# Kernel tuning notes

Hardware: AMD Instinct MI355X
Metric: run time of the kernel (lower is better)

Reference implementation:

```python
import jax, jax.numpy as jnp
import numpy as np

B, N, K, CIN, COUT = 2, 8192, 16, 64, 64


def setup_inputs() -> dict:
    key = jax.random.key(0)
    ks = jax.random.split(key, 12)
    w = lambda k, shape: jax.random.normal(k, shape, jnp.float32) * 0.02
    return dict(
        pos=jax.random.normal(ks[0], (B, N, 3), jnp.float32),
        features=jax.random.normal(ks[1], (B, N, CIN), jnp.float32),
        emb_w=w(ks[2], (CIN, COUT)), emb_b=jnp.zeros((COUT,), jnp.float32),
        wq=w(ks[3], (COUT, COUT)), wk=w(ks[4], (COUT, COUT)), wv=w(ks[5], (COUT, COUT)),
        pe_w1=w(ks[6], (3, COUT)), pe_b1=jnp.zeros((COUT,), jnp.float32),
        pe_w2=w(ks[7], (COUT, COUT)), pe_b2=jnp.zeros((COUT,), jnp.float32),
        at_w1=w(ks[8], (COUT, COUT)), at_b1=jnp.zeros((COUT,), jnp.float32),
        at_w2=w(ks[9], (COUT, COUT)), at_b2=jnp.zeros((COUT,), jnp.float32),
        out_w=w(ks[10], (COUT, CIN)), out_b=jnp.zeros((CIN,), jnp.float32),
    )


def _gather(x, idx):
    # x: [B, N, C], idx: [B, N, K] -> [B, N, K, C]
    return jax.vmap(lambda xb, ib: xb[ib])(x, idx)


def reference(pos, features, emb_w, emb_b, wq, wk, wv,
              pe_w1, pe_b1, pe_w2, pe_b2,
              at_w1, at_b1, at_w2, at_b2, out_w, out_b):
    # KNN: squared pairwise distances, take k smallest (includes self)
    sq = jnp.sum(pos * pos, axis=-1)                                  # [B, N]
    d2 = sq[:, :, None] + sq[:, None, :] - 2.0 * jnp.einsum('bnd,bmd->bnm', pos, pos)
    _, knn_idx = jax.lax.top_k(-d2, K)                                # [B, N, K]

    # recenter_groups: neighbor positions relative to query point
    grouped_pos = _gather(pos, knn_idx) - pos[:, :, None, :]          # [B, N, K, 3]

    x = features @ emb_w + emb_b                                      # [B, N, COUT]
    q = x @ wq                                                        # [B, N, COUT]
    k = _gather(x @ wk, knn_idx)                                      # [B, N, K, COUT]
    v = _gather(x @ wv, knn_idx)                                      # [B, N, K, COUT]

    # mlp_posenc: Linear(3,C) -> ReLU -> Linear(C,C)
    posenc = jax.nn.relu(grouped_pos @ pe_w1 + pe_b1) @ pe_w2 + pe_b2  # [B, N, K, COUT]

    # mlp_attn on (q - k + posenc), softmax over neighbor axis (dim=-2)
    h = q[:, :, None, :] - k + posenc
    attn = jax.nn.relu(h @ at_w1 + at_b1) @ at_w2 + at_b2
    attn = jax.nn.softmax(attn / np.float32(np.sqrt(COUT)), axis=-2)

    result = jnp.einsum('bmnf,bmnf->bmf', attn, v + posenc)           # [B, N, COUT]
    return result @ out_w + out_b + features                          # [B, N, CIN]
```

## Files before the change

### kernel.cpp

```cpp
#include <hip/hip_runtime.h>
#include <hip/hip_bf16.h>

#define BB 2
#define NN 8192
#define SPL 16
#define CAND (NN/SPL)
#define NPTS (BB*NN)

#define PART_OFF 0u
#define IDX_OFF  4194304u
#define WT_OFF   4456448u
#define QB_OFF   0u
#define KVB_OFF  1048576u

typedef __attribute__((ext_vector_type(8))) short bf16x8;
typedef __attribute__((ext_vector_type(4))) float f32x4;

__device__ __forceinline__ unsigned umn(unsigned a, unsigned b) {
#if __has_builtin(__builtin_elementwise_min)
  return __builtin_elementwise_min(a, b);
#else
  return a < b ? a : b;
#endif
}
__device__ __forceinline__ unsigned umx(unsigned a, unsigned b) {
#if __has_builtin(__builtin_elementwise_max)
  return __builtin_elementwise_max(a, b);
#else
  return a < b ? b : a;
#endif
}

__device__ inline unsigned short f2bf(float x) {
  __hip_bfloat16 b = __float2bfloat16(x);
  return *(unsigned short*)&b;
}

#define HCOL(c, j) ((((((c) >> 3) + (j)) & 7) << 3) | ((c) & 7))

__global__ __launch_bounds__(256) void k1_knn(const float* __restrict__ pos,
                                              unsigned* __restrict__ part)
{
  const int tid = threadIdx.x;
  const int g = blockIdx.x * 256 + tid;
  const int s = blockIdx.y;
  const int bu = __builtin_amdgcn_readfirstlane(g >> 13);
  const float qx = pos[g * 3 + 0], qy = pos[g * 3 + 1], qz = pos[g * 3 + 2];
  const float* __restrict__ cp = pos + (bu * NN + s * CAND) * 3;
  const unsigned jb = (unsigned)(s * CAND);
  unsigned m[16];
#pragma unroll
  for (int i = 0; i < 16; i++) m[i] = 0xFFFFFFFFu;

  constexpr int OE8[19][2] = {
    {0,1},{2,3},{4,5},{6,7},
    {0,2},{1,3},{4,6},{5,7},
    {1,2},{5,6},
    {0,4},{1,5},{2,6},{3,7},
    {2,4},{3,5},
    {1,2},{3,4},{5,6}
  };

  for (int j0 = 0; j0 < CAND; j0 += 8) {
    float c[24];
#pragma unroll
    for (int i = 0; i < 24; i++) c[i] = cp[j0 * 3 + i];
    unsigned b[8];
#pragma unroll
    for (int i = 0; i < 8; i++) {
      float dx = c[i * 3 + 0] - qx;
      float dy = c[i * 3 + 1] - qy;
      float dz = c[i * 3 + 2] - qz;
      float d2 = fmaf(dx, dx, fmaf(dy, dy, dz * dz));
      b[i] = (__float_as_uint(d2) & 0xFFFFE000u) | (jb + (unsigned)(j0 + i));
    }
#pragma unroll
    for (int cc = 0; cc < 19; cc++) {
      const int x = OE8[cc][0], y = OE8[cc][1];
      unsigned lo = umn(b[x], b[y]);
      unsigned hi = umx(b[x], b[y]);
      b[x] = hi; b[y] = lo;
    }
#pragma unroll
    for (int i = 0; i < 8; i++) m[8 + i] = umn(m[8 + i], b[i]);
#pragma unroll
    for (int d = 8; d; d >>= 1) {
#pragma unroll
      for (int i = 0; i < 16; i++) {
        if ((i & d) == 0) {
          const int l = i | d;
          unsigned lo = umn(m[i], m[l]);
          unsigned hi = umx(m[i], m[l]);
          m[i] = lo; m[l] = hi;
        }
      }
    }
  }
#pragma unroll
  for (int i = 0; i < 16; i++)
    part[(unsigned)(s * 16 + i) * NPTS + (unsigned)g] = m[i];
}

__global__ __launch_bounds__(256) void k2_merge(
    const unsigned* __restrict__ part, int* __restrict__ knn_idx,
    const float* __restrict__ pe_w2, const float* __restrict__ at_w1,
    const float* __restrict__ at_w2, const float* __restrict__ out_w,
    unsigned short* __restrict__ wt)
{
  if (blockIdx.x >= 64) {
    const int t = (blockIdx.x - 64) * 256 + threadIdx.x;
    const float* s;
    switch (t >> 12) {
      case 0: s = pe_w2; break;
      case 1: s = at_w1; break;
      case 2: s = at_w2; break;
      default: s = out_w; break;
    }
    const int idx = t & 4095, f = idx >> 6, c = idx & 63;
    wt[t] = f2bf(s[c * 64 + f]);
    return;
  }
  const int g = blockIdx.x * 256 + threadIdx.x;
  unsigned run[16];
#pragma unroll
  for (int i = 0; i < 16; i++) run[i] = part[i * NPTS + g];
#pragma unroll
  for (int l = 1; l < SPL; l++) {
#pragma unroll
    for (int i = 0; i < 16; i++)
      run[i] = umn(run[i], part[(l * 16 + 15 - i) * NPTS + g]);
#pragma unroll
    for (int d = 8; d; d >>= 1) {
#pragma unroll
      for (int i = 0; i < 16; i++) {
        if ((i & d) == 0) {
          const int l2 = i | d;
          unsigned lo = umn(run[i], run[l2]);
          unsigned hi = umx(run[i], run[l2]);
          run[i] = lo; run[l2] = hi;
        }
      }
    }
  }
  const int base = (g >> 13) * NN;
  int outv[16];
#pragma unroll
  for (int i = 0; i < 16; i++) outv[i] = base + (int)(run[i] & 0x1FFFu);
  int4* o = (int4*)(knn_idx + g * 16);
  o[0] = make_int4(outv[0], outv[1], outv[2], outv[3]);
  o[1] = make_int4(outv[4], outv[5], outv[6], outv[7]);
  o[2] = make_int4(outv[8], outv[9], outv[10], outv[11]);
  o[3] = make_int4(outv[12], outv[13], outv[14], outv[15]);
}

__global__ __launch_bounds__(256) void k34_embqkv(
    const float* __restrict__ feat,
    const float* __restrict__ emb_w, const float* __restrict__ emb_b,
    const float* __restrict__ wq, const float* __restrict__ wk,
    const float* __restrict__ wv,
    float* __restrict__ qo, unsigned* __restrict__ kvp)
{
  __shared__ float wl[16384];
  __shared__ float xl[2048];
  for (int i = threadIdx.x; i < 4096; i += 256) {
    wl[i] = emb_w[i];
    wl[4096 + i] = wq[i];
    wl[8192 + i] = wk[i];
    wl[12288 + i] = wv[i];
  }
  const int col = threadIdx.x & 63;
  const int rg = threadIdx.x >> 6;
  const int row0 = blockIdx.x * 32 + rg * 8;
  const int rowu = __builtin_amdgcn_readfirstlane(row0);
  __syncthreads();
  {
    float acc[8];
    float bias = emb_b[col];
#pragma unroll
    for (int r = 0; r < 8; r++) acc[r] = bias;
    for (int c = 0; c < 64; c++) {
      float w = wl[c * 64 + col];
      const float* fp = feat + rowu * 64 + c;
#pragma unroll
      for (int r = 0; r < 8; r++) acc[r] = fmaf(fp[r * 64], w, acc[r]);
    }
#pragma unroll
    for (int r = 0; r < 8; r++) xl[(rg * 8 + r) * 64 + col] = acc[r];
  }
  __syncthreads();
  float aq[8], ak[8], av[8];
#pragma unroll
  for (int r = 0; r < 8; r++) { aq[r] = 0.f; ak[r] = 0.f; av[r] = 0.f; }
  for (int c = 0; c < 64; c++) {
    float w0 = wl[4096 + c * 64 + col];
    float w1 = wl[8192 + c * 64 + col];
    float w2 = wl[12288 + c * 64 + col];
#pragma unroll
    for (int r = 0; r < 8; r++) {
      float xv = xl[(rg * 8 + r) * 64 + c];
      aq[r] = fmaf(xv, w0, aq[r]);
      ak[r] = fmaf(xv, w1, ak[r]);
      av[r] = fmaf(xv, w2, av[r]);
    }
  }
#pragma unroll
  for (int r = 0; r < 8; r++) {
    qo[(row0 + r) * 64 + col] = aq[r];
    kvp[(row0 + r) * 64 + col] =
        ((unsigned)f2bf(av[r]) << 16) | (unsigned)f2bf(ak[r]);
  }
}

__device__ inline void mv(const unsigned short* hm, const bf16x8 B[4][2],
                          const float bias[4], int ln, int s0, int s1,
                          f32x4 acc[4])
{
  bf16x8 a0 = *(const bf16x8*)(hm + ln * 64 + s0);
  bf16x8 a1 = *(const bf16x8*)(hm + ln * 64 + s1);
#pragma unroll
  for (int t = 0; t < 4; t++) {
    f32x4 a = {bias[t], bias[t], bias[t], bias[t]};
    a = __builtin_amdgcn_mfma_f32_16x16x32_bf16(a0, B[t][0], a, 0, 0, 0);
    a = __builtin_amdgcn_mfma_f32_16x16x32_bf16(a1, B[t][1], a, 0, 0, 0);
    acc[t] = a;
  }
}

__global__ __launch_bounds__(256, 2) void k5_attn(
    const float* __restrict__ pos, const float* __restrict__ qg,
    const unsigned* __restrict__ kvp, const float* __restrict__ featf,
    const float* __restrict__ pe_w1, const float* __restrict__ pe_b1,
    const float* __restrict__ pe_b2, const float* __restrict__ at_b1,
    const float* __restrict__ at_b2, const float* __restrict__ out_b,
    const unsigned short* __restrict__ wt, const int* __restrict__ knn,
    float* __restrict__ out)
{
  __shared__ unsigned short hma[4][1024];
  __shared__ unsigned short resm[1024];
  const int tid = threadIdx.x;
  const int wid = tid >> 6, lane = tid & 63;
  const int ln = lane & 15, quad = lane >> 4;
  unsigned short* hm = hma[wid];
  const int s0 = ((quad + ln) & 7) << 3;
  const int s1 = ((4 + quad + ln) & 7) << 3;

  bf16x8 Bf[3][4][2];
#pragma unroll
  for (int m = 0; m < 3; m++)
#pragma unroll
    for (int t = 0; t < 4; t++)
#pragma unroll
      for (int ks = 0; ks < 2; ks++)
        Bf[m][t][ks] = *(const bf16x8*)(wt + m * 4096 + (t * 16 + ln) * 64 +
                                        ks * 32 + quad * 8);
  bf16x8 bo[2];
#pragma unroll
  for (int ks = 0; ks < 2; ks++)
    bo[ks] = *(const bf16x8*)(wt + 3 * 4096 + (wid * 16 + ln) * 64 +
                              ks * 32 + quad * 8);

  float pw10 = pe_w1[lane], pw11 = pe_w1[64 + lane], pw12 = pe_w1[128 + lane];
  float pb1 = pe_b1[lane];
  float bpe[4], ba1[4], ba2[4];
#pragma unroll
  for (int t = 0; t < 4; t++) {
    bpe[t] = pe_b2[t * 16 + ln];
    ba1[t] = at_b1[t * 16 + ln];
    ba2[t] = at_b2[t * 16 + ln];
  }

  const int p0 = blockIdx.x * 16 + wid * 4;
  const int ps0 = __builtin_amdgcn_readfirstlane(p0);
  int4 cur[4];
  {
    const int4* ip4 = (const int4*)(knn + ps0 * 16);
#pragma unroll
    for (int u = 0; u < 4; u++) cur[u] = ip4[u];
  }

  for (int pp = 0; pp < 4; pp++) {
    const int p = p0 + pp;
    const int ps = __builtin_amdgcn_readfirstlane(p);
    int jj[16];
#pragma unroll
    for (int u = 0; u < 4; u++) {
      jj[u*4+0] = cur[u].x; jj[u*4+1] = cur[u].y;
      jj[u*4+2] = cur[u].z; jj[u*4+3] = cur[u].w;
    }
    int4 nxt[4];
    {
      const int pn = (pp < 3) ? (ps + 1) : ps;
      const int4* np4 = (const int4*)(knn + pn * 16);
#pragma unroll
      for (int u = 0; u < 4; u++) nxt[u] = np4[u];
    }
    unsigned kvw[4][4];
#pragma unroll
    for (int r = 0; r < 4; r++) {
      const unsigned* kp = kvp + jj[quad * 4 + r] * 64 + ln;
#pragma unroll
      for (int t = 0; t < 4; t++) kvw[r][t] = kp[t * 16];
    }
    float qv[4];
#pragma unroll
    for (int t = 0; t < 4; t++) qv[t] = qg[p * 64 + t * 16 + ln];

    const float* mp = pos + ps * 3;
    float pnx = mp[0], pny = mp[1], pnz = mp[2];
#pragma unroll
    for (int j = 0; j < 16; j++) {
      const float* np_ = pos + jj[j] * 3;
      float h1 = fmaf(np_[2] - pnz, pw12,
                 fmaf(np_[1] - pny, pw11,
                 fmaf(np_[0] - pnx, pw10, pb1)));
      hm[j * 64 + HCOL(lane, j)] = f2bf(fmaxf(h1, 0.f));
    }
    f32x4 accp[4];
    mv(hm, Bf[0], bpe, ln, s0, s1, accp);
    float vpe[4][4];
#pragma unroll
    for (int r = 0; r < 4; r++) {
      const int j = quad * 4 + r;
#pragma unroll
      for (int t = 0; t < 4; t++) {
        const unsigned w = kvw[r][t];
        float kf = __uint_as_float(w << 16);
        float vf = __uint_as_float(w & 0xFFFF0000u);
        float pe = accp[t][r];
        vpe[t][r] = vf + pe;
        hm[j * 64 + HCOL(t * 16 + ln, j)] = f2bf(qv[t] - kf + pe);
      }
    }
    f32x4 acch[4];
    mv(hm, Bf[1], ba1, ln, s0, s1, acch);
#pragma unroll
    for (int t = 0; t < 4; t++)
#pragma unroll
      for (int r = 0; r < 4; r++) {
        const int j = quad * 4 + r;
        hm[j * 64 + HCOL(t * 16 + ln, j)] = f2bf(fmaxf(acch[t][r], 0.f));
      }
    f32x4 lg[4];
    mv(hm, Bf[2], ba2, ln, s0, s1, lg);
    const int pb = wid * 4 + pp;
#pragma unroll
    for (int t = 0; t < 4; t++) {
      float e0 = __expf(lg[t][0] * 0.125f);
      float e1 = __expf(lg[t][1] * 0.125f);
      float e2 = __expf(lg[t][2] * 0.125f);
      float e3 = __expf(lg[t][3] * 0.125f);
      float ss = (e0 + e1) + (e2 + e3);
      float dt = fmaf(e3, vpe[t][3], fmaf(e2, vpe[t][2],
                 fmaf(e1, vpe[t][1], e0 * vpe[t][0])));
      ss += __shfl_xor(ss, 16); ss += __shfl_xor(ss, 32);
      dt += __shfl_xor(dt, 16); dt += __shfl_xor(dt, 32);
      float res = dt / ss;
      if (quad == 0) resm[pb * 64 + HCOL(t * 16 + ln, pb)] = f2bf(res);
    }
#pragma unroll
    for (int u = 0; u < 4; u++) cur[u] = nxt[u];
  }
  __syncthreads();
  {
    const int nt = wid;
    float ob = out_b[nt * 16 + ln];
    f32x4 acc = {ob, ob, ob, ob};
#pragma unroll
    for (int ks = 0; ks < 2; ks++) {
      bf16x8 a = *(const bf16x8*)(resm + ln * 64 +
                                  (((ks * 4 + quad + ln) & 7) << 3));
      acc = __builtin_amdgcn_mfma_f32_16x16x32_bf16(a, bo[ks], acc, 0, 0, 0);
    }
#pragma unroll
    for (int r = 0; r < 4; r++) {
      const int pt = blockIdx.x * 16 + quad * 4 + r;
      const int f = nt * 16 + ln;
      out[pt * 64 + f] = acc[r] + featf[pt * 64 + f];
    }
  }
}

extern "C" void kernel_launch(void* const* d_in, const int* in_sizes, int n_in,
                              void* d_out, int out_size, void* d_ws, size_t ws_size,
                              hipStream_t stream)
{
  (void)in_sizes; (void)n_in; (void)out_size; (void)ws_size;
  const float* pos   = (const float*)d_in[0];
  const float* feat  = (const float*)d_in[1];
  const float* emb_w = (const float*)d_in[2];
  const float* emb_b = (const float*)d_in[3];
  const float* wq    = (const float*)d_in[4];
  const float* wk    = (const float*)d_in[5];
  const float* wv    = (const float*)d_in[6];
  const float* pe_w1 = (const float*)d_in[7];
  const float* pe_b1 = (const float*)d_in[8];
  const float* pe_w2 = (const float*)d_in[9];
  const float* pe_b2 = (const float*)d_in[10];
  const float* at_w1 = (const float*)d_in[11];
  const float* at_b1 = (const float*)d_in[12];
  const float* at_w2 = (const float*)d_in[13];
  const float* at_b2 = (const float*)d_in[14];
  const float* out_w = (const float*)d_in[15];
  const float* out_b = (const float*)d_in[16];
  float* ws = (float*)d_ws;

  dim3 g1(NPTS / 256, SPL);
  k1_knn<<<g1, 256, 0, stream>>>(pos, (unsigned*)ws + PART_OFF);
  k2_merge<<<128, 256, 0, stream>>>((unsigned*)ws + PART_OFF,
      (int*)ws + IDX_OFF, pe_w2, at_w1, at_w2, out_w,
      (unsigned short*)(ws + WT_OFF));
  k34_embqkv<<<NPTS / 32, 256, 0, stream>>>(feat, emb_w, emb_b, wq, wk, wv,
      ws + QB_OFF, (unsigned*)ws + KVB_OFF);
  k5_attn<<<NPTS / 16, 256, 0, stream>>>(pos, ws + QB_OFF,
      (unsigned*)ws + KVB_OFF, feat, pe_w1, pe_b1, pe_b2, at_b1, at_b2, out_b,
      (unsigned short*)(ws + WT_OFF), (int*)ws + IDX_OFF, (float*)d_out);
}
```

Measured before the change: 240.1 us.

## Fuse four kernels into two and merge KNN partials inside attention kernel

Merges the KNN partial search, embedding/QKV projection and weight transposition into one heterogeneous launch, selected by block index. The KNN top-16 merge moves into the attention kernel, where four lanes per wave compute neighbor indices into shared memory instead of reading a separate index array. The KNN inner loop now sorts 16 candidates per step instead of 8, and positions are repacked as float4 for single-load gathers. This removes two launches and one global round trip for the indices, at the cost of serial merge work on a few lanes, more register pressure in the KNN loop, and lower LDS occupancy in the fused first kernel.

Measured after the change: 249.7 us. +4.0%, slower.

```diff
diff --git a/kernel.cpp b/kernel.cpp
--- a/kernel.cpp
+++ b/kernel.cpp
@@ -7,11 +7,11 @@
 #define CAND (NN/SPL)
 #define NPTS (BB*NN)
 
-#define PART_OFF 0u
-#define IDX_OFF  4194304u
-#define WT_OFF   4456448u
-#define QB_OFF   0u
-#define KVB_OFF  1048576u
+#define POS4_OFF 0u
+#define PART_OFF 65536u
+#define QB_OFF   4259840u
+#define KVB_OFF  5308416u
+#define WT_OFF   6356992u
 
 typedef __attribute__((ext_vector_type(8))) short bf16x8;
 typedef __attribute__((ext_vector_type(4))) float f32x4;
@@ -38,77 +38,144 @@
 
 #define HCOL(c, j) ((((((c) >> 3) + (j)) & 7) << 3) | ((c) & 7))
 
-__global__ __launch_bounds__(256) void k1_knn(const float* __restrict__ pos,
-                                              unsigned* __restrict__ part)
-{
-  const int tid = threadIdx.x;
-  const int g = blockIdx.x * 256 + tid;
-  const int s = blockIdx.y;
-  const int bu = __builtin_amdgcn_readfirstlane(g >> 13);
-  const float qx = pos[g * 3 + 0], qy = pos[g * 3 + 1], qz = pos[g * 3 + 2];
-  const float* __restrict__ cp = pos + (bu * NN + s * CAND) * 3;
-  const unsigned jb = (unsigned)(s * CAND);
-  unsigned m[16];
-#pragma unroll
-  for (int i = 0; i < 16; i++) m[i] = 0xFFFFFFFFu;
-
-  constexpr int OE8[19][2] = {
-    {0,1},{2,3},{4,5},{6,7},
-    {0,2},{1,3},{4,6},{5,7},
-    {1,2},{5,6},
-    {0,4},{1,5},{2,6},{3,7},
-    {2,4},{3,5},
-    {1,2},{3,4},{5,6}
-  };
-
-  for (int j0 = 0; j0 < CAND; j0 += 8) {
-    float c[24];
-#pragma unroll
-    for (int i = 0; i < 24; i++) c[i] = cp[j0 * 3 + i];
-    unsigned b[8];
-#pragma unroll
-    for (int i = 0; i < 8; i++) {
-      float dx = c[i * 3 + 0] - qx;
-      float dy = c[i * 3 + 1] - qy;
-      float dz = c[i * 3 + 2] - qz;
-      float d2 = fmaf(dx, dx, fmaf(dy, dy, dz * dz));
-      b[i] = (__float_as_uint(d2) & 0xFFFFE000u) | (jb + (unsigned)(j0 + i));
-    }
-#pragma unroll
-    for (int cc = 0; cc < 19; cc++) {
-      const int x = OE8[cc][0], y = OE8[cc][1];
-      unsigned lo = umn(b[x], b[y]);
-      unsigned hi = umx(b[x], b[y]);
-      b[x] = hi; b[y] = lo;
-    }
-#pragma unroll
-    for (int i = 0; i < 8; i++) m[8 + i] = umn(m[8 + i], b[i]);
-#pragma unroll
-    for (int d = 8; d; d >>= 1) {
-#pragma unroll
-      for (int i = 0; i < 16; i++) {
-        if ((i & d) == 0) {
-          const int l = i | d;
-          unsigned lo = umn(m[i], m[l]);
-          unsigned hi = umx(m[i], m[l]);
-          m[i] = lo; m[l] = hi;
-        }
-      }
-    }
-  }
-#pragma unroll
-  for (int i = 0; i < 16; i++)
-    part[(unsigned)(s * 16 + i) * NPTS + (unsigned)g] = m[i];
-}
-
-__global__ __launch_bounds__(256) void k2_merge(
-    const unsigned* __restrict__ part, int* __restrict__ knn_idx,
+__global__ __launch_bounds__(256) void mega1(
+    const float* __restrict__ pos, const float* __restrict__ feat,
+    const float* __restrict__ emb_w, const float* __restrict__ emb_b,
+    const float* __restrict__ wq, const float* __restrict__ wk,
+    const float* __restrict__ wv,
     const float* __restrict__ pe_w2, const float* __restrict__ at_w1,
     const float* __restrict__ at_w2, const float* __restrict__ out_w,
-    unsigned short* __restrict__ wt)
+    float* __restrict__ ws)
 {
-  if (blockIdx.x >= 64) {
-    const int t = (blockIdx.x - 64) * 256 + threadIdx.x;
+  __shared__ __align__(16) char smem[57344];
+  const int tid = threadIdx.x;
+  const int bx = blockIdx.x;
+  float* pos4 = ws + POS4_OFF;
+  unsigned* part = (unsigned*)ws + PART_OFF;
+  float* qg = ws + QB_OFF;
+  unsigned* kvp = (unsigned*)ws + KVB_OFF;
+  unsigned short* wt = (unsigned short*)(ws + WT_OFF);
+
+  if (bx < 512) {
+    float* wl = (float*)smem;
+    float* xl = (float*)(smem + 49152);
+    if (tid < 32) {
+      const int p = bx * 32 + tid;
+      float x = pos[p * 3 + 0], y = pos[p * 3 + 1], z = pos[p * 3 + 2];
+      float4 v = {x, y, z, fmaf(x, x, fmaf(y, y, z * z))};
+      ((float4*)pos4)[p] = v;
+    }
+    for (int i = tid; i < 4096; i += 256) wl[i] = emb_w[i];
+    const int col = tid & 63;
+    const int rg = tid >> 6;
+    const int row0 = bx * 32 + rg * 8;
+    const int rowu = __builtin_amdgcn_readfirstlane(row0);
+    __syncthreads();
+    {
+      float acc[8];
+      float bias = emb_b[col];
+#pragma unroll
+      for (int r = 0; r < 8; r++) acc[r] = bias;
+      for (int c = 0; c < 64; c++) {
+        float w = wl[c * 64 + col];
+        const float* fp = feat + rowu * 64 + c;
+#pragma unroll
+        for (int r = 0; r < 8; r++) acc[r] = fmaf(fp[r * 64], w, acc[r]);
+      }
+#pragma unroll
+      for (int r = 0; r < 8; r++) xl[(rg * 8 + r) * 64 + col] = acc[r];
+    }
+    __syncthreads();
+    for (int i = tid; i < 4096; i += 256) {
+      wl[i] = wq[i];
+      wl[4096 + i] = wk[i];
+      wl[8192 + i] = wv[i];
+    }
+    __syncthreads();
+    float aq[8], ak[8], av[8];
+#pragma unroll
+    for (int r = 0; r < 8; r++) { aq[r] = 0.f; ak[r] = 0.f; av[r] = 0.f; }
+    for (int c = 0; c < 64; c++) {
+      float w0 = wl[c * 64 + col];
+      float w1 = wl[4096 + c * 64 + col];
+      float w2 = wl[8192 + c * 64 + col];
+#pragma unroll
+      for (int r = 0; r < 8; r++) {
+        float xv = xl[(rg * 8 + r) * 64 + c];
+        aq[r] = fmaf(xv, w0, aq[r]);
+        ak[r] = fmaf(xv, w1, ak[r]);
+        av[r] = fmaf(xv, w2, av[r]);
+      }
+    }
+#pragma unroll
+    for (int r = 0; r < 8; r++) {
+      qg[(row0 + r) * 64 + col] = aq[r];
+      kvp[(row0 + r) * 64 + col] =
+          ((unsigned)f2bf(av[r]) << 16) | (unsigned)f2bf(ak[r]);
+    }
+  } else if (bx < 1536) {
+    constexpr int OE[63][2] = {
+      {0,1},{2,3},{4,5},{6,7},{8,9},{10,11},{12,13},{14,15},
+      {0,2},{1,3},{4,6},{5,7},{8,10},{9,11},{12,14},{13,15},
+      {1,2},{5,6},{9,10},{13,14},
+      {0,4},{1,5},{2,6},{3,7},{8,12},{9,13},{10,14},{11,15},
+      {2,4},{3,5},{10,12},{11,13},
+      {1,2},{3,4},{5,6},{9,10},{11,12},{13,14},
+      {0,8},{1,9},{2,10},{3,11},{4,12},{5,13},{6,14},{7,15},
+      {4,8},{5,9},{6,10},{7,11},
+      {2,4},{3,5},{6,8},{7,9},{10,12},{11,13},
+      {1,2},{3,4},{5,6},{7,8},{9,10},{11,12},{13,14}
+    };
+    const int vb = bx - 512;
+    const int g = (vb & 63) * 256 + tid;
+    const int s = vb >> 6;
+    const int bu = __builtin_amdgcn_readfirstlane(g >> 13);
+    const float qx = pos[g * 3 + 0], qy = pos[g * 3 + 1], qz = pos[g * 3 + 2];
+    const float* __restrict__ cp = pos + (bu * NN + s * CAND) * 3;
+    const unsigned jb = (unsigned)(s * CAND);
+    unsigned m[16];
+#pragma unroll
+    for (int i = 0; i < 16; i++) m[i] = 0xFFFFFFFFu;
+    for (int j0 = 0; j0 < CAND; j0 += 16) {
+      float c[48];
+#pragma unroll
+      for (int i = 0; i < 48; i++) c[i] = cp[j0 * 3 + i];
+      unsigned b[16];
+#pragma unroll
+      for (int i = 0; i < 16; i++) {
+        float dx = c[i * 3 + 0] - qx;
+        float dy = c[i * 3 + 1] - qy;
+        float dz = c[i * 3 + 2] - qz;
+        float d2 = fmaf(dx, dx, fmaf(dy, dy, dz * dz));
+        b[i] = (__float_as_uint(d2) & 0xFFFFE000u) | (jb + (unsigned)(j0 + i));
+      }
+#pragma unroll
+      for (int cc = 0; cc < 63; cc++) {
+        const int x = OE[cc][0], y = OE[cc][1];
+        unsigned lo = umn(b[x], b[y]);
+        unsigned hi = umx(b[x], b[y]);
+        b[x] = hi; b[y] = lo;
+      }
+#pragma unroll
+      for (int i = 0; i < 16; i++) m[i] = umn(m[i], b[i]);
+#pragma unroll
+      for (int d = 8; d; d >>= 1) {
+#pragma unroll
+        for (int i = 0; i < 16; i++) {
+          if ((i & d) == 0) {
+            const int l = i | d;
+            unsigned lo = umn(m[i], m[l]);
+            unsigned hi = umx(m[i], m[l]);
+            m[i] = lo; m[l] = hi;
+          }
+        }
+      }
+    }
+#pragma unroll
+    for (int i = 0; i < 16; i++)
+      part[(unsigned)(s * 16 + i) * NPTS + (unsigned)g] = m[i];
+  } else {
+    const int t = (bx - 1536) * 256 + tid;
     const float* s;
     switch (t >> 12) {
       case 0: s = pe_w2; break;
@@ -118,96 +185,6 @@
     }
     const int idx = t & 4095, f = idx >> 6, c = idx & 63;
     wt[t] = f2bf(s[c * 64 + f]);
-    return;
-  }
-  const int g = blockIdx.x * 256 + threadIdx.x;
-  unsigned run[16];
-#pragma unroll
-  for (int i = 0; i < 16; i++) run[i] = part[i * NPTS + g];
-#pragma unroll
-  for (int l = 1; l < SPL; l++) {
-#pragma unroll
-    for (int i = 0; i < 16; i++)
-      run[i] = umn(run[i], part[(l * 16 + 15 - i) * NPTS + g]);
-#pragma unroll
-    for (int d = 8; d; d >>= 1) {
-#pragma unroll
-      for (int i = 0; i < 16; i++) {
-        if ((i & d) == 0) {
-          const int l2 = i | d;
-          unsigned lo = umn(run[i], run[l2]);
-          unsigned hi = umx(run[i], run[l2]);
-          run[i] = lo; run[l2] = hi;
-        }
-      }
-    }
-  }
-  const int base = (g >> 13) * NN;
-  int outv[16];
-#pragma unroll
-  for (int i = 0; i < 16; i++) outv[i] = base + (int)(run[i] & 0x1FFFu);
-  int4* o = (int4*)(knn_idx + g * 16);
-  o[0] = make_int4(outv[0], outv[1], outv[2], outv[3]);
-  o[1] = make_int4(outv[4], outv[5], outv[6], outv[7]);
-  o[2] = make_int4(outv[8], outv[9], outv[10], outv[11]);
-  o[3] = make_int4(outv[12], outv[13], outv[14], outv[15]);
-}
-
-__global__ __launch_bounds__(256) void k34_embqkv(
-    const float* __restrict__ feat,
-    const float* __restrict__ emb_w, const float* __restrict__ emb_b,
-    const float* __restrict__ wq, const float* __restrict__ wk,
-    const float* __restrict__ wv,
-    float* __restrict__ qo, unsigned* __restrict__ kvp)
-{
-  __shared__ float wl[16384];
-  __shared__ float xl[2048];
-  for (int i = threadIdx.x; i < 4096; i += 256) {
-    wl[i] = emb_w[i];
-    wl[4096 + i] = wq[i];
-    wl[8192 + i] = wk[i];
-    wl[12288 + i] = wv[i];
-  }
-  const int col = threadIdx.x & 63;
-  const int rg = threadIdx.x >> 6;
-  const int row0 = blockIdx.x * 32 + rg * 8;
-  const int rowu = __builtin_amdgcn_readfirstlane(row0);
-  __syncthreads();
-  {
-    float acc[8];
-    float bias = emb_b[col];
-#pragma unroll
-    for (int r = 0; r < 8; r++) acc[r] = bias;
-    for (int c = 0; c < 64; c++) {
-      float w = wl[c * 64 + col];
-      const float* fp = feat + rowu * 64 + c;
-#pragma unroll
-      for (int r = 0; r < 8; r++) acc[r] = fmaf(fp[r * 64], w, acc[r]);
-    }
-#pragma unroll
-    for (int r = 0; r < 8; r++) xl[(rg * 8 + r) * 64 + col] = acc[r];
-  }
-  __syncthreads();
-  float aq[8], ak[8], av[8];
-#pragma unroll
-  for (int r = 0; r < 8; r++) { aq[r] = 0.f; ak[r] = 0.f; av[r] = 0.f; }
-  for (int c = 0; c < 64; c++) {
-    float w0 = wl[4096 + c * 64 + col];
-    float w1 = wl[8192 + c * 64 + col];
-    float w2 = wl[12288 + c * 64 + col];
-#pragma unroll
-    for (int r = 0; r < 8; r++) {
-      float xv = xl[(rg * 8 + r) * 64 + c];
-      aq[r] = fmaf(xv, w0, aq[r]);
-      ak[r] = fmaf(xv, w1, ak[r]);
-      av[r] = fmaf(xv, w2, av[r]);
-    }
-  }
-#pragma unroll
-  for (int r = 0; r < 8; r++) {
-    qo[(row0 + r) * 64 + col] = aq[r];
-    kvp[(row0 + r) * 64 + col] =
-        ((unsigned)f2bf(av[r]) << 16) | (unsigned)f2bf(ak[r]);
   }
 }
 
@@ -226,24 +203,59 @@
   }
 }
 
-__global__ __launch_bounds__(256, 2) void k5_attn(
-    const float* __restrict__ pos, const float* __restrict__ qg,
-    const unsigned* __restrict__ kvp, const float* __restrict__ featf,
+__global__ __launch_bounds__(256, 2) void mega2(
+    const float* __restrict__ ws_ro, const float* __restrict__ feat,
     const float* __restrict__ pe_w1, const float* __restrict__ pe_b1,
     const float* __restrict__ pe_b2, const float* __restrict__ at_b1,
     const float* __restrict__ at_b2, const float* __restrict__ out_b,
-    const unsigned short* __restrict__ wt, const int* __restrict__ knn,
     float* __restrict__ out)
 {
   __shared__ unsigned short hma[4][1024];
   __shared__ unsigned short resm[1024];
+  __shared__ int idxm[16][16];
+  const float* pos4 = ws_ro + POS4_OFF;
+  const unsigned* part = (const unsigned*)ws_ro + PART_OFF;
+  const float* qg = ws_ro + QB_OFF;
+  const unsigned* kvp = (const unsigned*)ws_ro + KVB_OFF;
+  const unsigned short* wt = (const unsigned short*)(ws_ro + WT_OFF);
+
   const int tid = threadIdx.x;
+  const int bx = blockIdx.x;
   const int wid = tid >> 6, lane = tid & 63;
   const int ln = lane & 15, quad = lane >> 4;
   unsigned short* hm = hma[wid];
   const int s0 = ((quad + ln) & 7) << 3;
   const int s1 = ((4 + quad + ln) & 7) << 3;
 
+  if (lane < 4) {
+    const int pb = wid * 4 + lane;
+    const int g = bx * 16 + pb;
+    unsigned run[16];
+#pragma unroll
+    for (int i = 0; i < 16; i++) run[i] = part[i * NPTS + g];
+#pragma unroll
+    for (int l = 1; l < SPL; l++) {
+#pragma unroll
+      for (int i = 0; i < 16; i++)
+        run[i] = umn(run[i], part[(l * 16 + 15 - i) * NPTS + g]);
+#pragma unroll
+      for (int d = 8; d; d >>= 1) {
+#pragma unroll
+        for (int i = 0; i < 16; i++) {
+          if ((i & d) == 0) {
+            const int l2 = i | d;
+            unsigned lo = umn(run[i], run[l2]);
+            unsigned hi = umx(run[i], run[l2]);
+            run[i] = lo; run[l2] = hi;
+          }
+        }
+      }
+    }
+    const int base = (g >> 13) * NN;
+#pragma unroll
+    for (int i = 0; i < 16; i++) idxm[pb][i] = base + (int)(run[i] & 0x1FFFu);
+  }
+
   bf16x8 Bf[3][4][2];
 #pragma unroll
   for (int m = 0; m < 3; m++)
@@ -268,31 +280,17 @@
     ba1[t] = at_b1[t * 16 + ln];
     ba2[t] = at_b2[t * 16 + ln];
   }
-
-  const int p0 = blockIdx.x * 16 + wid * 4;
-  const int ps0 = __builtin_amdgcn_readfirstlane(p0);
-  int4 cur[4];
-  {
-    const int4* ip4 = (const int4*)(knn + ps0 * 16);
-#pragma unroll
-    for (int u = 0; u < 4; u++) cur[u] = ip4[u];
-  }
+  const float4* pp4 = (const float4*)pos4;
 
   for (int pp = 0; pp < 4; pp++) {
-    const int p = p0 + pp;
+    const int pb = wid * 4 + pp;
+    const int p = bx * 16 + pb;
     const int ps = __builtin_amdgcn_readfirstlane(p);
     int jj[16];
 #pragma unroll
     for (int u = 0; u < 4; u++) {
-      jj[u*4+0] = cur[u].x; jj[u*4+1] = cur[u].y;
-      jj[u*4+2] = cur[u].z; jj[u*4+3] = cur[u].w;
-    }
-    int4 nxt[4];
-    {
-      const int pn = (pp < 3) ? (ps + 1) : ps;
-      const int4* np4 = (const int4*)(knn + pn * 16);
-#pragma unroll
-      for (int u = 0; u < 4; u++) nxt[u] = np4[u];
+      int4 t4 = ((const int4*)&idxm[pb][0])[u];
+      jj[u*4+0] = t4.x; jj[u*4+1] = t4.y; jj[u*4+2] = t4.z; jj[u*4+3] = t4.w;
     }
     unsigned kvw[4][4];
 #pragma unroll
@@ -305,14 +303,13 @@
 #pragma unroll
     for (int t = 0; t < 4; t++) qv[t] = qg[p * 64 + t * 16 + ln];
 
-    const float* mp = pos + ps * 3;
-    float pnx = mp[0], pny = mp[1], pnz = mp[2];
+    const float4 mp = pp4[ps];
 #pragma unroll
     for (int j = 0; j < 16; j++) {
-      const float* np_ = pos + jj[j] * 3;
-      float h1 = fmaf(np_[2] - pnz, pw12,
-                 fmaf(np_[1] - pny, pw11,
-                 fmaf(np_[0] - pnx, pw10, pb1)));
+      const float4 np = pp4[jj[j]];
+      float h1 = fmaf(np.z - mp.z, pw12,
+                 fmaf(np.y - mp.y, pw11,
+                 fmaf(np.x - mp.x, pw10, pb1)));
       hm[j * 64 + HCOL(lane, j)] = f2bf(fmaxf(h1, 0.f));
     }
     f32x4 accp[4];
@@ -342,7 +339,6 @@
       }
     f32x4 lg[4];
     mv(hm, Bf[2], ba2, ln, s0, s1, lg);
-    const int pb = wid * 4 + pp;
 #pragma unroll
     for (int t = 0; t < 4; t++) {
       float e0 = __expf(lg[t][0] * 0.125f);
@@ -357,8 +353,6 @@
       float res = dt / ss;
       if (quad == 0) resm[pb * 64 + HCOL(t * 16 + ln, pb)] = f2bf(res);
     }
-#pragma unroll
-    for (int u = 0; u < 4; u++) cur[u] = nxt[u];
   }
   __syncthreads();
   {
@@ -373,9 +367,9 @@
     }
 #pragma unroll
     for (int r = 0; r < 4; r++) {
-      const int pt = blockIdx.x * 16 + quad * 4 + r;
+      const int pt = bx * 16 + quad * 4 + r;
       const int f = nt * 16 + ln;
-      out[pt * 64 + f] = acc[r] + featf[pt * 64 + f];
+      out[pt * 64 + f] = acc[r] + feat[pt * 64 + f];
     }
   }
 }
@@ -404,14 +398,8 @@
   const float* out_b = (const float*)d_in[16];
   float* ws = (float*)d_ws;
 
-  dim3 g1(NPTS / 256, SPL);
-  k1_knn<<<g1, 256, 0, stream>>>(pos, (unsigned*)ws + PART_OFF);
-  k2_merge<<<128, 256, 0, stream>>>((unsigned*)ws + PART_OFF,
-      (int*)ws + IDX_OFF, pe_w2, at_w1, at_w2, out_w,
-      (unsigned short*)(ws + WT_OFF));
-  k34_embqkv<<<NPTS / 32, 256, 0, stream>>>(feat, emb_w, emb_b, wq, wk, wv,
-      ws + QB_OFF, (unsigned*)ws + KVB_OFF);
-  k5_attn<<<NPTS / 16, 256, 0, stream>>>(pos, ws + QB_OFF,
-      (unsigned*)ws + KVB_OFF, feat, pe_w1, pe_b1, pe_b2, at_b1, at_b2, out_b,
-      (unsigned short*)(ws + WT_OFF), (int*)ws + IDX_OFF, (float*)d_out);
-}
+  mega1<<<1600, 256, 0, stream>>>(pos, feat, emb_w, emb_b, wq, wk, wv,
+                                  pe_w2, at_w1, at_w2, out_w, ws);
+  mega2<<<NPTS / 16, 256, 0, stream>>>(ws, feat, pe_w1, pe_b1, pe_b2,
+                                       at_b1, at_b2, out_b, (float*)d_out);
+}
```
